# Kernel optimization log

Hardware: AMD Instinct MI355X
Metric: run time of the kernel (lower is better)

Reference implementation:

```python
import jax, jax.numpy as jnp
import numpy as np

RATIO = 4
K_TOP = 2

def setup_inputs() -> dict:
    key = jax.random.key(0)
    k1, k2 = jax.random.split(key)
    B, C, H, W = 4, 128, 128, 128
    N_low = (H // RATIO) * (W // RATIO)
    v_high_feat = jax.random.normal(k1, (B, C, H, W), dtype=jnp.float32)
    coarse_attn_map = jax.random.normal(k2, (B, N_low, N_low), dtype=jnp.float32)
    return {"v_high_feat": v_high_feat, "coarse_attn_map": coarse_attn_map}

def reference(v_high_feat, coarse_attn_map):
    ratio, k = RATIO, K_TOP
    B, C, H, W = v_high_feat.shape
    H_low, W_low = H // ratio, W // ratio
    N_high, N_low = H * W, H_low * W_low
    r2 = ratio * ratio

    # [B, N_high, C]
    v_seq = v_high_feat.reshape(B, C, N_high).transpose(0, 2, 1)

    # top-k over coarse attention rows: [B, N_low, k]
    topk_values, topk_idx = jax.lax.top_k(coarse_attn_map, k)

    # low-res 2d coords of top-k keys, scaled to high-res top-left corners
    tl_row = (topk_idx // W_low) * ratio  # [B, N_low, k]
    tl_col = (topk_idx % W_low) * ratio

    # r x r patch offsets: [r2, 2]
    dr, dc = jnp.meshgrid(jnp.arange(ratio), jnp.arange(ratio), indexing='ij')
    drow, dcol = dr.reshape(-1), dc.reshape(-1)

    # flattened high-res indices per (low query, sample, patch cell): [B, N_low, k*r2]
    sparse_row = tl_row[..., None] + drow  # [B, N_low, k, r2]
    sparse_col = tl_col[..., None] + dcol
    sparse_1d = (sparse_row * W + sparse_col).reshape(B, N_low, k * r2)

    # each high-res query maps to its containing low-res cell: [N_high]
    qr, qc = jnp.meshgrid(jnp.arange(H), jnp.arange(W), indexing='ij')
    low_idx = ((qr // ratio) * W_low + (qc // ratio)).reshape(N_high)

    # broadcast low-res sample indices/weights to every high-res query
    final_idx = sparse_1d[:, low_idx, :]  # [B, N_high, k*r2]

    # gather sampled values: [B, N_high, k*r2, C]
    batch_idx = jnp.arange(B)[:, None, None]
    v_sparse = v_seq[batch_idx, final_idx]

    # softmax weights over k samples, gathered to high-res queries
    w_low = jax.nn.softmax(topk_values, axis=-1)  # [B, N_low, k]
    w_high = w_low[:, low_idx, :]                 # [B, N_high, k]

    v_r = v_sparse.reshape(B, N_high, k, r2, C)
    w = (w_high / r2)[..., None, None]            # [B, N_high, k, 1, 1]
    warped_seq = (v_r * w).sum(axis=(2, 3))       # [B, N_high, C]

    return warped_seq.transpose(0, 2, 1).reshape(B, C, H, W)
```

## Files before the change

kernel.cpp:

```cpp
#include <hip/hip_runtime.h>
#include <float.h>

#define B_ 4
#define C_ 128
#define H_ 128
#define W_ 128
#define WL_ 32
#define NL_ 1024

__global__ __launch_bounds__(256) void k_fusedA(const float* __restrict__ v,
                                                const float* __restrict__ attn,
                                                float* __restrict__ S,
                                                int2* __restrict__ tmap,
                                                float2* __restrict__ wmap) {
    if (blockIdx.x < 512) {
        int plane = blockIdx.x;
        const float* vp = v + (size_t)plane * (H_ * W_);
        float* Sp = S + (size_t)plane * NL_;
        int tid = threadIdx.x;
        #pragma unroll
        for (int rep = 0; rep < 4; ++rep) {
            int cell = rep * 256 + tid;
            int cr = cell >> 5, cc = cell & 31;
            const float* rp = vp + (cr * 4) * W_ + cc * 4;
            float s = 0.f;
            #pragma unroll
            for (int r = 0; r < 4; ++r) {
                float4 u = *(const float4*)(rp + r * W_);
                s += u.x + u.y + u.z + u.w;
            }
            Sp[cell] = s;
        }
    } else {
        int lane = threadIdx.x & 63;
        int wv   = threadIdx.x >> 6;
        int row  = (blockIdx.x - 512) * 4 + wv;
        const float4* p = (const float4*)(attn + (size_t)row * NL_);

        float v0 = -FLT_MAX, v1 = -FLT_MAX;
        int   i0 = 0x7fffffff, i1 = 0x7fffffff;

        #pragma unroll
        for (int s = 0; s < 4; ++s) {
            float4 u = p[lane + 64 * s];
            int j = 4 * (lane + 64 * s);
            float vals[4] = {u.x, u.y, u.z, u.w};
            #pragma unroll
            for (int t = 0; t < 4; ++t) {
                float a = vals[t];
                int   ji = j + t;
                if (a > v0)      { v1 = v0; i1 = i0; v0 = a; i0 = ji; }
                else if (a > v1) { v1 = a; i1 = ji; }
            }
        }

        #pragma unroll
        for (int off = 32; off >= 1; off >>= 1) {
            float ov0 = __shfl_xor(v0, off, 64);
            int   oi0 = __shfl_xor(i0, off, 64);
            float ov1 = __shfl_xor(v1, off, 64);
            int   oi1 = __shfl_xor(i1, off, 64);
            bool a_first = (v0 > ov0) || (v0 == ov0 && i0 < oi0);
            float n0, n1; int m0, m1;
            if (a_first) {
                n0 = v0; m0 = i0;
                bool s2 = (v1 > ov0) || (v1 == ov0 && i1 < oi0);
                n1 = s2 ? v1 : ov0; m1 = s2 ? i1 : oi0;
            } else {
                n0 = ov0; m0 = oi0;
                bool s2 = (v0 > ov1) || (v0 == ov1 && i0 < oi1);
                n1 = s2 ? v0 : ov1; m1 = s2 ? i0 : oi1;
            }
            v0 = n0; i0 = m0; v1 = n1; i1 = m1;
        }

        if (lane == 0) {
            float e  = expf(v1 - v0);
            float w0 = 1.f / (1.f + e);
            tmap[row] = make_int2(i0, i1);
            wmap[row] = make_float2(w0, 1.f - w0);
        }
    }
}

__global__ __launch_bounds__(256) void k_out(const float* __restrict__ S,
                                             const int2* __restrict__ tmap,
                                             const float2* __restrict__ wmap,
                                             float* __restrict__ out) {
    int item = blockIdx.x * 256 + threadIdx.x;
    int wb = item & 31;
    int ht = (item >> 5) & 31;
    int c  = (item >> 10) & 127;
    int b  = item >> 17;
    int row = b * NL_ + ht * WL_ + wb;

    int2   t = tmap[row];
    float2 w = wmap[row];
    const float* Sp = S + ((size_t)(b * C_ + c)) * NL_;
    float val = (w.x * Sp[t.x] + w.y * Sp[t.y]) * 0.0625f;

    float4 o4 = make_float4(val, val, val, val);
    float* op = out + ((size_t)(b * C_ + c) * H_ + ht * 4) * W_ + wb * 4;
    #pragma unroll
    for (int r = 0; r < 4; ++r)
        *(float4*)(op + r * W_) = o4;
}

extern "C" void kernel_launch(void* const* d_in, const int* in_sizes, int n_in,
                              void* d_out, int out_size, void* d_ws, size_t ws_size,
                              hipStream_t stream) {
    const float* v    = (const float*)d_in[0];
    const float* attn = (const float*)d_in[1];
    float* out = (float*)d_out;

    char* base = (char*)d_ws;
    float*  S    = (float*)base;
    int2*   tmap = (int2*)(base + (size_t)B_ * C_ * NL_ * 4);
    float2* wmap = (float2*)(base + (size_t)B_ * C_ * NL_ * 4 + 4096 * sizeof(int2));

    k_fusedA<<<512 + 1024, 256, 0, stream>>>(v, attn, S, tmap, wmap);
    k_out<<<(B_ * C_ * WL_ * WL_) / 256, 256, 0, stream>>>(S, tmap, wmap, out);
}
```

Measured before the change: 98.13 us.

## Fuse patch pooling with output expansion per plane using shared memory

```diff
diff --git a/kernel.cpp b/kernel.cpp
--- a/kernel.cpp
+++ b/kernel.cpp
@@ -8,102 +8,93 @@
 #define WL_ 32
 #define NL_ 1024
 
-__global__ __launch_bounds__(256) void k_fusedA(const float* __restrict__ v,
-                                                const float* __restrict__ attn,
-                                                float* __restrict__ S,
-                                                int2* __restrict__ tmap,
-                                                float2* __restrict__ wmap) {
-    if (blockIdx.x < 512) {
-        int plane = blockIdx.x;
-        const float* vp = v + (size_t)plane * (H_ * W_);
-        float* Sp = S + (size_t)plane * NL_;
-        int tid = threadIdx.x;
+__global__ __launch_bounds__(256) void k_top2(const float* __restrict__ attn,
+                                              int2* __restrict__ tmap,
+                                              float2* __restrict__ wmap) {
+    int lane = threadIdx.x & 63;
+    int wv   = threadIdx.x >> 6;
+    int row  = blockIdx.x * 4 + wv;
+    const float4* p = (const float4*)(attn + (size_t)row * NL_);
+
+    float v0 = -FLT_MAX, v1 = -FLT_MAX;
+    int   i0 = 0x7fffffff, i1 = 0x7fffffff;
+
+    #pragma unroll
+    for (int s = 0; s < 4; ++s) {
+        float4 u = p[lane + 64 * s];
+        int j = 4 * (lane + 64 * s);
+        float vals[4] = {u.x, u.y, u.z, u.w};
         #pragma unroll
-        for (int rep = 0; rep < 4; ++rep) {
-            int cell = rep * 256 + tid;
-            int cr = cell >> 5, cc = cell & 31;
-            const float* rp = vp + (cr * 4) * W_ + cc * 4;
-            float s = 0.f;
-            #pragma unroll
-            for (int r = 0; r < 4; ++r) {
-                float4 u = *(const float4*)(rp + r * W_);
-                s += u.x + u.y + u.z + u.w;
-            }
-            Sp[cell] = s;
+        for (int t = 0; t < 4; ++t) {
+            float a = vals[t];
+            int   ji = j + t;
+            if (a > v0)      { v1 = v0; i1 = i0; v0 = a; i0 = ji; }
+            else if (a > v1) { v1 = a; i1 = ji; }
         }
-    } else {
-        int lane = threadIdx.x & 63;
-        int wv   = threadIdx.x >> 6;
-        int row  = (blockIdx.x - 512) * 4 + wv;
-        const float4* p = (const float4*)(attn + (size_t)row * NL_);
+    }
 
-        float v0 = -FLT_MAX, v1 = -FLT_MAX;
-        int   i0 = 0x7fffffff, i1 = 0x7fffffff;
+    #pragma unroll
+    for (int off = 32; off >= 1; off >>= 1) {
+        float ov0 = __shfl_xor(v0, off, 64);
+        int   oi0 = __shfl_xor(i0, off, 64);
+        float ov1 = __shfl_xor(v1, off, 64);
+        int   oi1 = __shfl_xor(i1, off, 64);
+        bool a_first = (v0 > ov0) || (v0 == ov0 && i0 < oi0);
+        float n0, n1; int m0, m1;
+        if (a_first) {
+            n0 = v0; m0 = i0;
+            bool s2 = (v1 > ov0) || (v1 == ov0 && i1 < oi0);
+            n1 = s2 ? v1 : ov0; m1 = s2 ? i1 : oi0;
+        } else {
+            n0 = ov0; m0 = oi0;
+            bool s2 = (v0 > ov1) || (v0 == ov1 && i0 < oi1);
+            n1 = s2 ? v0 : ov1; m1 = s2 ? i0 : oi1;
+        }
+        v0 = n0; i0 = m0; v1 = n1; i1 = m1;
+    }
 
-        #pragma unroll
-        for (int s = 0; s < 4; ++s) {
-            float4 u = p[lane + 64 * s];
-            int j = 4 * (lane + 64 * s);
-            float vals[4] = {u.x, u.y, u.z, u.w};
-            #pragma unroll
-            for (int t = 0; t < 4; ++t) {
-                float a = vals[t];
-                int   ji = j + t;
-                if (a > v0)      { v1 = v0; i1 = i0; v0 = a; i0 = ji; }
-                else if (a > v1) { v1 = a; i1 = ji; }
-            }
-        }
-
-        #pragma unroll
-        for (int off = 32; off >= 1; off >>= 1) {
-            float ov0 = __shfl_xor(v0, off, 64);
-            int   oi0 = __shfl_xor(i0, off, 64);
-            float ov1 = __shfl_xor(v1, off, 64);
-            int   oi1 = __shfl_xor(i1, off, 64);
-            bool a_first = (v0 > ov0) || (v0 == ov0 && i0 < oi0);
-            float n0, n1; int m0, m1;
-            if (a_first) {
-                n0 = v0; m0 = i0;
-                bool s2 = (v1 > ov0) || (v1 == ov0 && i1 < oi0);
-                n1 = s2 ? v1 : ov0; m1 = s2 ? i1 : oi0;
-            } else {
-                n0 = ov0; m0 = oi0;
-                bool s2 = (v0 > ov1) || (v0 == ov1 && i0 < oi1);
-                n1 = s2 ? v0 : ov1; m1 = s2 ? i0 : oi1;
-            }
-            v0 = n0; i0 = m0; v1 = n1; i1 = m1;
-        }
-
-        if (lane == 0) {
-            float e  = expf(v1 - v0);
-            float w0 = 1.f / (1.f + e);
-            tmap[row] = make_int2(i0, i1);
-            wmap[row] = make_float2(w0, 1.f - w0);
-        }
+    if (lane == 0) {
+        float e  = expf(v1 - v0);
+        float w0 = 1.f / (1.f + e);
+        tmap[row] = make_int2(i0, i1);
+        wmap[row] = make_float2(w0, 1.f - w0);
     }
 }
 
-__global__ __launch_bounds__(256) void k_out(const float* __restrict__ S,
-                                             const int2* __restrict__ tmap,
-                                             const float2* __restrict__ wmap,
-                                             float* __restrict__ out) {
-    int item = blockIdx.x * 256 + threadIdx.x;
-    int wb = item & 31;
-    int ht = (item >> 5) & 31;
-    int c  = (item >> 10) & 127;
-    int b  = item >> 17;
-    int row = b * NL_ + ht * WL_ + wb;
+__global__ __launch_bounds__(1024) void k_plane(const float* __restrict__ v,
+                                                const int2* __restrict__ tmap,
+                                                const float2* __restrict__ wmap,
+                                                float* __restrict__ out) {
+    __shared__ float S_l[NL_];
+    int plane = blockIdx.x;
+    int b   = plane >> 7;
+    int tid = threadIdx.x;
 
-    int2   t = tmap[row];
-    float2 w = wmap[row];
-    const float* Sp = S + ((size_t)(b * C_ + c)) * NL_;
-    float val = (w.x * Sp[t.x] + w.y * Sp[t.y]) * 0.0625f;
+    {
+        int cr = tid >> 5, cc = tid & 31;
+        const float* rp = v + (size_t)plane * (H_ * W_) + (cr * 4) * W_ + cc * 4;
+        float s = 0.f;
+        #pragma unroll
+        for (int r = 0; r < 4; ++r) {
+            float4 u = *(const float4*)(rp + r * W_);
+            s += u.x + u.y + u.z + u.w;
+        }
+        S_l[tid] = s;
+    }
+    __syncthreads();
 
-    float4 o4 = make_float4(val, val, val, val);
-    float* op = out + ((size_t)(b * C_ + c) * H_ + ht * 4) * W_ + wb * 4;
-    #pragma unroll
-    for (int r = 0; r < 4; ++r)
-        *(float4*)(op + r * W_) = o4;
+    {
+        int2   t = tmap[b * NL_ + tid];
+        float2 w = wmap[b * NL_ + tid];
+        float val = (w.x * S_l[t.x] + w.y * S_l[t.y]) * 0.0625f;
+
+        int ht = tid >> 5, wb = tid & 31;
+        float4 o4 = make_float4(val, val, val, val);
+        float* op = out + ((size_t)plane * H_ + ht * 4) * W_ + wb * 4;
+        #pragma unroll
+        for (int r = 0; r < 4; ++r)
+            *(float4*)(op + r * W_) = o4;
+    }
 }
 
 extern "C" void kernel_launch(void* const* d_in, const int* in_sizes, int n_in,
@@ -114,10 +105,9 @@
     float* out = (float*)d_out;
 
     char* base = (char*)d_ws;
-    float*  S    = (float*)base;
-    int2*   tmap = (int2*)(base + (size_t)B_ * C_ * NL_ * 4);
-    float2* wmap = (float2*)(base + (size_t)B_ * C_ * NL_ * 4 + 4096 * sizeof(int2));
+    int2*   tmap = (int2*)base;
+    float2* wmap = (float2*)(base + 4096 * sizeof(int2));
 
-    k_fusedA<<<512 + 1024, 256, 0, stream>>>(v, attn, S, tmap, wmap);
-    k_out<<<(B_ * C_ * WL_ * WL_) / 256, 256, 0, stream>>>(S, tmap, wmap, out);
+    k_top2<<<1024, 256, 0, stream>>>(attn, tmap, wmap);
+    k_plane<<<B_ * C_, 1024, 0, stream>>>(v, tmap, wmap, out);
 }
```

Result: faster. 95.37 us (median of 2 runs) (-2.8%).
